# Kernel optimization log

Measured on AMD Instinct MI355X. Metric: run time of the kernel, lower is better.

The kernel has to match this reference:

```python
import jax, jax.numpy as jnp
import numpy as np

B, J, C = 256, 21, 256   # batch, joints, in_dim
H, D = 8, 256            # heads, out_dim (=hidden)
L, K = 2, 8              # layers, knn_k


def _knn_idx(coords, k):
    # coords: (B,J,3). Squared distances give same ordering as cdist p=2.
    d2 = jnp.sum((coords[:, :, None, :] - coords[:, None, :, :]) ** 2, axis=-1)  # (B,J,J)
    order = jnp.argsort(d2, axis=-1)
    return order[..., 1:k + 1]  # drop self -> (B,J,K)


def _mhgat(x, nbr_idx, wq, wk, wv, wp):
    b, j, _ = x.shape
    q = (x @ wq).reshape(b, j, H, D)
    k = (x @ wk).reshape(b, j, H, D)
    v = (x @ wv).reshape(b, j, H, D)
    bi = jnp.arange(b)[:, None, None]
    k_nbr = k[bi, nbr_idx]  # (B,J,K,H,D) gather of neighbor keys
    v_nbr = v[bi, nbr_idx]  # (B,J,K,H,D)
    attn = jnp.einsum('bjhd,bjkhd->bjkh', q, k_nbr) / np.float32(np.sqrt(D))
    attn = jax.nn.leaky_relu(attn, negative_slope=0.2)
    attn = jax.nn.softmax(attn, axis=2)  # over K neighbors
    out = jnp.einsum('bjkh,bjkhd->bjhd', attn, v_nbr).reshape(b, j, H * D)
    return out @ wp  # (B,J,hidden)


def setup_inputs() -> dict:
    key = jax.random.key(0)
    ks = jax.random.split(key, 9)
    s_in = 1.0 / np.sqrt(C)
    s_hd = 1.0 / np.sqrt(H * D)
    s_h = 1.0 / np.sqrt(D)
    joint_feats = jax.random.normal(ks[0], (B, J, C), jnp.float32)
    # layer-stacked weights (in_dim == hidden == 256 so both layers stack)
    wq = jax.random.normal(ks[1], (L, C, H * D), jnp.float32) * s_in
    wk = jax.random.normal(ks[2], (L, C, H * D), jnp.float32) * s_in
    wv = jax.random.normal(ks[3], (L, C, H * D), jnp.float32) * s_in
    wp = jax.random.normal(ks[4], (L, H * D, D), jnp.float32) * s_hd
    ws = jax.random.normal(ks[5], (L, C, D), jnp.float32) * s_in
    wskip0 = jax.random.normal(ks[6], (C, D), jnp.float32) * s_in
    fc_w = jax.random.normal(ks[7], (D, 3), jnp.float32) * s_h
    fc_b = jax.random.normal(ks[8], (3,), jnp.float32) * s_h
    return {"joint_feats": joint_feats, "wq": wq, "wk": wk, "wv": wv,
            "wp": wp, "ws": ws, "wskip0": wskip0, "fc_w": fc_w, "fc_b": fc_b}


def reference(joint_feats, wq, wk, wv, wp, ws, wskip0, fc_w, fc_b):
    h0 = joint_feats
    h = h0
    stats = []
    for l in range(L):
        nbr_idx = _knn_idx(jax.lax.stop_gradient(h[..., :3]), K)  # dynamic kNN graph
        out = _mhgat(h, nbr_idx, wq[l], wk[l], wv[l], wp[l])
        h = jax.nn.relu(out + h @ ws[l] + h0 @ wskip0)
        stats.append(jnp.abs(h).mean())
    coords = h @ fc_w + fc_b
    alphas = jnp.mean(jnp.stack(stats))
    return coords, alphas
```

## Files before the change

kernel.cpp:

```cpp
#include <hip/hip_runtime.h>
#include <hip/hip_bf16.h>
#include <math.h>
#include <type_traits>

namespace {
constexpr int Bb = 256, Jj = 21, Cc = 256, Hh = 8, Dd = 256;
constexpr int Mrows = Bb * Jj;
constexpr int HD    = Hh * Dd;
constexpr int QKVN  = 3 * HD;
constexpr int KNN   = 8;
constexpr int KFUSE = HD + Cc + Cc;

constexpr size_t OFF_QKV   = 0;
constexpr size_t OFF_T     = OFF_QKV   + (size_t)Mrows*QKVN*2;
constexpr size_t OFF_ATT   = OFF_T     + (size_t)Mrows*HD*4;
constexpr size_t OFF_GT    = OFF_ATT   + (size_t)Mrows*HD*2;
constexpr size_t OFF_JFB   = OFF_GT    + (size_t)HD*768*2;
constexpr size_t OFF_JFH   = OFF_JFB   + (size_t)Mrows*Cc*2;
constexpr size_t OFF_JFL   = OFF_JFH   + (size_t)Mrows*Cc*2;
constexpr size_t OFF_JFD   = OFF_JFL   + (size_t)Mrows*Cc*2;
constexpr size_t OFF_H1B   = OFF_JFD   + (size_t)Mrows*Cc*2;
constexpr size_t OFF_H2F   = OFF_H1B   + (size_t)Mrows*Cc*2;
constexpr size_t OFF_WQKVT = OFF_H2F   + (size_t)Mrows*Cc*4;
constexpr size_t OFF_FBT   = OFF_WQKVT + (size_t)2*QKVN*Cc*2;
constexpr size_t OFF_WVP   = OFF_FBT   + (size_t)2*Cc*KFUSE*2;
constexpr size_t OFF_VPROJ = OFF_WVP   + (size_t)Cc*24*4;
constexpr size_t OFF_WSUM  = OFF_VPROJ + (size_t)Mrows*24*4;
constexpr size_t OFF_CRD   = OFF_WSUM  + (size_t)Cc*4*4;
constexpr size_t OFF_NBR0  = OFF_CRD   + (size_t)Mrows*4*4;
constexpr size_t OFF_NBR1  = OFF_NBR0  + (size_t)Mrows*KNN*4;
constexpr size_t OFF_STAT  = OFF_NBR1  + (size_t)Mrows*KNN*4;
}

typedef short short8 __attribute__((ext_vector_type(8)));
typedef _Float16 half8 __attribute__((ext_vector_type(8)));
typedef _Float16 half4v __attribute__((ext_vector_type(4)));
typedef unsigned short u16x8 __attribute__((ext_vector_type(8)));
typedef float f32x4 __attribute__((ext_vector_type(4)));

__device__ __forceinline__ unsigned short f2bf(float x) {
    unsigned int u = __float_as_uint(x);
    u = u + 0x7fffu + ((u >> 16) & 1u);
    return (unsigned short)(u >> 16);
}
__device__ __forceinline__ float bf2f(unsigned short b) {
    return __uint_as_float(((unsigned int)b) << 16);
}

__device__ __forceinline__ void knn_body(int b, const float* __restrict__ src,
                                         int ld, int* __restrict__ nbr,
                                         float (*cs)[3]) {
    int t = threadIdx.x;
    if (t < Jj) {
        const float* p = src + (size_t)(b * Jj + t) * ld;
        cs[t][0] = p[0]; cs[t][1] = p[1]; cs[t][2] = p[2];
    }
    __syncthreads();
    if (t < Jj) {
        float x = cs[t][0], y = cs[t][1], z = cs[t][2];
        float d2[Jj];
        #pragma unroll
        for (int jj = 0; jj < Jj; ++jj) {
            float dx = x - cs[jj][0], dy = y - cs[jj][1], dz = z - cs[jj][2];
            d2[jj] = dx*dx + dy*dy + dz*dz;
        }
        unsigned int used = 0u;
        int out_base = (b * Jj + t) * KNN;
        #pragma unroll
        for (int r = 0; r <= KNN; ++r) {
            int best = -1; float bd = INFINITY;
            #pragma unroll
            for (int jj = 0; jj < Jj; ++jj)
                if (!((used >> jj) & 1u) && d2[jj] < bd) { bd = d2[jj]; best = jj; }
            used |= (1u << best);
            if (r > 0) nbr[out_base + r - 1] = best;
        }
    }
}

__global__ __launch_bounds__(256)
void mega_prep_kernel(const float* __restrict__ jf,
                      const float* __restrict__ wq, const float* __restrict__ wk,
                      const float* __restrict__ wv, const float* __restrict__ wp,
                      const float* __restrict__ wsw, const float* __restrict__ wsk,
                      unsigned short* __restrict__ wqkvT,
                      unsigned short* __restrict__ fbt, float* __restrict__ stats,
                      float* __restrict__ wsum,
                      unsigned short* __restrict__ jfb, _Float16* __restrict__ jfh,
                      _Float16* __restrict__ jfl, _Float16* __restrict__ jfd,
                      _Float16* __restrict__ GT, float* __restrict__ Wvp2,
                      int* __restrict__ nbr0) {
    __shared__ __align__(16) char sm[17408];
    int bid = blockIdx.x;
    int tidx = threadIdx.x;

    if (bid < 256) {
        int h = bid >> 5, rem = bid & 31;
        int m0 = (rem >> 2) * 32, n0 = (rem & 3) * 64;
        float (*As)[36] = (float(*)[36])sm;
        float (*Ws)[68] = (float(*)[68])(sm + 4608);
        int ty = tidx >> 4, tx = tidx & 15;
        float acc[2][4] = {};
        for (int kb = 0; kb < 256; kb += 32) {
            {
                int row = tidx >> 3, col = (tidx & 7) * 4;
                float4 v = *(const float4*)&wq[(size_t)(m0 + row)*HD + h*256 + kb + col];
                As[col+0][row] = v.x; As[col+1][row] = v.y;
                As[col+2][row] = v.z; As[col+3][row] = v.w;
                int row2 = tidx >> 2, col2 = (tidx & 3) * 8;
                float4 u0 = *(const float4*)&wk[(size_t)(n0 + row2)*HD + h*256 + kb + col2];
                float4 u1 = *(const float4*)&wk[(size_t)(n0 + row2)*HD + h*256 + kb + col2 + 4];
                Ws[col2+0][row2] = u0.x; Ws[col2+1][row2] = u0.y;
                Ws[col2+2][row2] = u0.z; Ws[col2+3][row2] = u0.w;
                Ws[col2+4][row2] = u1.x; Ws[col2+5][row2] = u1.y;
                Ws[col2+6][row2] = u1.z; Ws[col2+7][row2] = u1.w;
            }
            __syncthreads();
            #pragma unroll
            for (int kk = 0; kk < 32; ++kk) {
                float a0 = As[kk][ty*2], a1 = As[kk][ty*2 + 1];
                float4 bv = *(const float4*)&Ws[kk][tx*4];
                float b4[4] = {bv.x, bv.y, bv.z, bv.w};
                #pragma unroll
                for (int j = 0; j < 4; ++j) {
                    acc[0][j] += a0 * b4[j];
                    acc[1][j] += a1 * b4[j];
                }
            }
            __syncthreads();
        }
        #pragma unroll
        for (int j = 0; j < 4; ++j) {
            int n = h*256 + n0 + tx*4 + j;
            float g0 = acc[0][j], g1 = acc[1][j];
            _Float16 h0_ = (_Float16)g0, h1_ = (_Float16)g1;
            _Float16* base = &GT[(size_t)n*768 + m0 + ty*2];
            base[0]   = h0_;                          base[1]   = h1_;
            base[256] = (_Float16)(g0 * 0.0625f);     base[257] = (_Float16)(g1 * 0.0625f);
            base[512] = (_Float16)((g0 - (float)h0_) * 128.0f);
            base[513] = (_Float16)((g1 - (float)h1_) * 128.0f);
        }
    } else if (bid < 264) {
        int h = bid - 256;
        float (*wpc)[3] = (float(*)[3])sm;
        int t = tidx;
        const float* p = &wp[(size_t)(h*256 + t) * Cc];
        wpc[t][0] = p[0]; wpc[t][1] = p[1]; wpc[t][2] = p[2];
        __syncthreads();
        const float* vr = &wv[(size_t)t*HD + h*256];
        float a0=0, a1=0, a2=0;
        for (int d = 0; d < 256; ++d) {
            float v = vr[d];
            a0 += v*wpc[d][0]; a1 += v*wpc[d][1]; a2 += v*wpc[d][2];
        }
        float* o = &Wvp2[(size_t)t*24 + h*3];
        o[0]=a0; o[1]=a1; o[2]=a2;
    } else if (bid < 520) {
        knn_body(bid - 264, jf, Cc, nbr0, (float(*)[3])sm);
    } else if (bid == 520) {
        int e = tidx;
        float4 o;
        o.x = wsw[(size_t)e*Dd + 0] + wsk[(size_t)e*Dd + 0];
        o.y = wsw[(size_t)e*Dd + 1] + wsk[(size_t)e*Dd + 1];
        o.z = wsw[(size_t)e*Dd + 2] + wsk[(size_t)e*Dd + 2];
        o.w = 0.0f;
        *(float4*)&wsum[e*4] = o;
        if (e < 2) stats[e] = 0.0f;
    } else if (bid < 1865) {
        int i = (bid - 521) * 256 + tidx;
        float4 v = ((const float4*)jf)[i];
        float x[4] = {v.x, v.y, v.z, v.w};
        ushort4 ob; half4v oh, ol, od;
        #pragma unroll
        for (int u = 0; u < 4; ++u) {
            ((unsigned short*)&ob)[u] = f2bf(x[u]);
            _Float16 h = (_Float16)x[u];
            oh[u] = h;
            ol[u] = (_Float16)((x[u] - (float)h) * 16.0f);
            od[u] = (_Float16)(x[u] * 0.0078125f);
        }
        ((ushort4*)jfb)[i] = ob;
        ((half4v*)jfh)[i] = oh;
        ((half4v*)jfl)[i] = ol;
        ((half4v*)jfd)[i] = od;
    } else {
        int tt = bid - 1865;
        const float* src; unsigned short* dst;
        int ldin, ldout, tilesX, tile;
        constexpr size_t CH = (size_t)Cc * HD;
        if (tt < 3072) {
            int op = tt >> 9; tile = tt & 511; tilesX = 64;
            ldin = HD; ldout = Cc;
            const float* s3[3] = {wq, wk, wv};
            src = s3[op % 3] + (size_t)(op / 3) * CH;
            dst = wqkvT + (size_t)(op % 3) * HD * Cc + (size_t)(op / 3) * QKVN * Cc;
        } else if (tt < 4096) {
            int op = (tt - 3072) >> 9; tile = (tt - 3072) & 511; tilesX = 8;
            ldin = Cc; ldout = KFUSE;
            src = wp + (size_t)op * HD * Cc;
            dst = fbt + (size_t)op * Cc * KFUSE;
        } else {
            int q = tt - 4096; int op = q >> 6; tile = q & 63; tilesX = 8;
            ldin = Cc; ldout = KFUSE;
            const float* s4[4] = {wsw, wsw + (size_t)Cc * Cc, wsk, wsk};
            src = s4[op];
            dst = fbt + (size_t)(op & 1) * Cc * KFUSE + HD + (size_t)(op >> 1) * Cc;
        }
        int bx = tile % tilesX, by = tile / tilesX;
        int n0 = bx * 32, k0 = by * 32;
        float (*t)[33] = (float(*)[33])sm;
        int r = tidx >> 3, c4 = (tidx & 7) * 4;
        float4 v = *(const float4*)&src[(size_t)(k0 + r) * ldin + n0 + c4];
        t[r][c4+0] = v.x; t[r][c4+1] = v.y; t[r][c4+2] = v.z; t[r][c4+3] = v.w;
        __syncthreads();
        ushort4 o;
        o.x = f2bf(t[c4+0][r]); o.y = f2bf(t[c4+1][r]);
        o.z = f2bf(t[c4+2][r]); o.w = f2bf(t[c4+3][r]);
        *(ushort4*)&dst[(size_t)(n0 + r) * ldout + k0 + c4] = o;
    }
}

template<int BM, int BN, int BK, int NSEG, bool RELU_STATS, bool OUT_BF16, bool F16>
__device__ __forceinline__
void gemm_core(unsigned short* As, unsigned short* Bs, float* red,
               int bm, int bn,
               const unsigned short* __restrict__ A0, int lda0, int klen0,
               const unsigned short* __restrict__ A1, int lda1, int klen1,
               const unsigned short* __restrict__ A2, int lda2, int klen2,
               const unsigned short* __restrict__ Bt, int ldb,
               void* __restrict__ Cv, int ldc, float* __restrict__ stat) {
    constexpr int WM = BM/2, WN = BN/2;
    constexpr int MW = WM/16, NW = WN/16, KW = BK/32;
    constexpr int CHUNKA = BM*BK/8;
    constexpr int CHUNKB = BN*BK/8;
    constexpr int KB8 = BK/8;
    constexpr int SWZ = KB8 - 1;
    using frag = std::conditional_t<F16, half8, short8>;

    int tid = threadIdx.x;
    int wid = tid >> 6, lane = tid & 63;
    int wr = wid >> 1, wc = wid & 1;

    f32x4 acc[MW][NW];
    #pragma unroll
    for (int m = 0; m < MW; ++m)
        #pragma unroll
        for (int n = 0; n < NW; ++n)
            acc[m][n] = (f32x4){0.f, 0.f, 0.f, 0.f};

    const unsigned short* Aseg[3] = {A0, A1, A2};
    const int ldas[3] = {lda0, lda1, lda2};
    const int klens[3] = {klen0, klen1, klen2};

    int kglob = 0;
    for (int seg = 0; seg < NSEG; ++seg) {
        const unsigned short* A = Aseg[seg];
        const int lda = ldas[seg];
        const int klen = klens[seg];
        for (int k0 = 0; k0 < klen; k0 += BK) {
            #pragma unroll
            for (int it = 0; it < CHUNKA/256; ++it) {
                int c = tid + it*256;
                int row = c / KB8;
                int kp = (c % KB8) ^ (row & SWZ);
                __builtin_amdgcn_global_load_lds(
                    (const __attribute__((address_space(1))) unsigned int*)
                        (A + (size_t)(bm + row)*lda + k0 + kp*8),
                    (__attribute__((address_space(3))) unsigned int*)(As + c*8),
                    16, 0, 0);
            }
            #pragma unroll
            for (int it = 0; it < CHUNKB/256; ++it) {
                int c = tid + it*256;
                int row = c / KB8;
                int kp = (c % KB8) ^ (row & SWZ);
                __builtin_amdgcn_global_load_lds(
                    (const __attribute__((address_space(1))) unsigned int*)
                        (Bt + (size_t)(bn + row)*ldb + kglob + k0 + kp*8),
                    (__attribute__((address_space(3))) unsigned int*)(Bs + c*8),
                    16, 0, 0);
            }
            __syncthreads();
            #pragma unroll
            for (int kp = 0; kp < KW; ++kp) {
                frag af[MW], bf[NW];
                int cbase = kp*4 + (lane >> 4);
                #pragma unroll
                for (int m = 0; m < MW; ++m) {
                    int r = wr*WM + m*16 + (lane & 15);
                    af[m] = *(const frag*)&As[r*BK + ((cbase ^ (r & SWZ))*8)];
                }
                #pragma unroll
                for (int n = 0; n < NW; ++n) {
                    int r = wc*WN + n*16 + (lane & 15);
                    bf[n] = *(const frag*)&Bs[r*BK + ((cbase ^ (r & SWZ))*8)];
                }
                #pragma unroll
                for (int m = 0; m < MW; ++m)
                    #pragma unroll
                    for (int n = 0; n < NW; ++n) {
                        if constexpr (F16)
                            acc[m][n] = __builtin_amdgcn_mfma_f32_16x16x32_f16(
                                af[m], bf[n], acc[m][n], 0, 0, 0);
                        else
                            acc[m][n] = __builtin_amdgcn_mfma_f32_16x16x32_bf16(
                                af[m], bf[n], acc[m][n], 0, 0, 0);
                    }
            }
            __syncthreads();
        }
        kglob += klen;
    }

    int cr = (lane >> 4)*4, cc = lane & 15;
    float bsum = 0.0f;
    #pragma unroll
    for (int m = 0; m < MW; ++m)
        #pragma unroll
        for (int n = 0; n < NW; ++n)
            #pragma unroll
            for (int j = 0; j < 4; ++j) {
                float v = acc[m][n][j];
                if (RELU_STATS) { v = fmaxf(v, 0.0f); bsum += v; }
                size_t row = bm + wr*WM + m*16 + cr + j;
                size_t col = bn + wc*WN + n*16 + cc;
                if (OUT_BF16) ((unsigned short*)Cv)[row*ldc + col] = f2bf(v);
                else          ((float*)Cv)[row*ldc + col] = v;
            }
    if (RELU_STATS) {
        #pragma unroll
        for (int sft = 1; sft < 64; sft <<= 1) bsum += __shfl_xor(bsum, sft);
        if (lane == 0) red[wid] = bsum;
        __syncthreads();
        if (tid == 0) atomicAdd(stat, red[0] + red[1] + red[2] + red[3]);
    }
}

__global__ __launch_bounds__(256)
void combo_kernel(const unsigned short* __restrict__ jfb,
                  const unsigned short* __restrict__ wqkvT,
                  unsigned short* __restrict__ QKVb,
                  const _Float16* __restrict__ jfh, const _Float16* __restrict__ jfl,
                  const _Float16* __restrict__ jfd, const _Float16* __restrict__ GT,
                  float* __restrict__ Tm,
                  const float* __restrict__ jf, const float* __restrict__ Wvp2,
                  float* __restrict__ vproj) {
    __shared__ __align__(16) char smem[32784];
    unsigned short* As = (unsigned short*)smem;
    unsigned short* Bs = (unsigned short*)(smem + 16384);
    float* red = (float*)(smem + 32768);
    int x = blockIdx.x, y = blockIdx.y;
    if (y < 16) {
        int lb = x + 42*y;
        int nb = (lb & 7) * 84 + (lb >> 3);
        int sx = nb % 42, sy = nb / 42;
        gemm_core<128,128,64,1,false,true,false>(As, Bs, red, sx*128,
            2*HD + sy*128,
            jfb, Cc, Cc, jfb, Cc, 0, jfb, Cc, 0, wqkvT, Cc, QKVb, QKVN, nullptr);
    } else if (y < 32) {
        int lb = x + 42*(y - 16);
        int nb = (lb & 7) * 84 + (lb >> 3);
        int sx = nb / 16, sy = nb % 16;
        gemm_core<128,128,64,3,false,false,true>(As, Bs, red, sx*128, sy*128,
            (const unsigned short*)jfh, Cc, Cc, (const unsigned short*)jfl, Cc, Cc,
            (const unsigned short*)jfd, Cc, Cc, (const unsigned short*)GT, 768,
            Tm, HD, nullptr);
    } else {
        int q = (y - 32) * 42 + x;
        float (*hr)[256] = (float(*)[256])smem;
        float* wl = (float*)(smem + 8192);
        int t = threadIdx.x;
        int j0 = q * 8;
        #pragma unroll
        for (int i = 0; i < 6; ++i)
            *(float4*)&wl[t*4 + i*1024] = *(const float4*)&Wvp2[t*4 + i*1024];
        {
            int r = t >> 5, c = (t & 31) * 8;
            const float* src = &jf[(size_t)(j0 + r)*Cc + c];
            *(float4*)&hr[r][c]   = *(const float4*)src;
            *(float4*)&hr[r][c+4] = *(const float4*)(src + 4);
        }
        __syncthreads();
        int r = t >> 5, o = t & 31;
        if (o < 24) {
            float a = 0.0f;
            for (int e = 0; e < 256; ++e) a += hr[r][e] * wl[e*24 + o];
            vproj[(size_t)(j0 + r)*24 + o] = a;
        }
    }
}

__global__ __launch_bounds__(256)
void qkv1_kernel(const unsigned short* __restrict__ h1b,
                 const unsigned short* __restrict__ wqkvT1,
                 unsigned short* __restrict__ QKVb) {
    __shared__ __align__(16) unsigned short As[128*64];
    __shared__ __align__(16) unsigned short Bs[128*64];
    __shared__ float red[4];
    int lb = blockIdx.x + 42*blockIdx.y;
    int nb = (lb & 7) * 252 + (lb >> 3);
    int sx = nb % 42, sy = nb / 42;
    gemm_core<128,128,64,1,false,true,false>(
        As, Bs, red, sx*128, sy*128,
        h1b, Cc, Cc, h1b, Cc, 0, h1b, Cc, 0, wqkvT1, Cc, QKVb, QKVN, nullptr);
}

template<bool OUT_BF16, bool DO_KNN>
__global__ __launch_bounds__(256)
void fused_kernel(const unsigned short* __restrict__ att,
                  const unsigned short* __restrict__ hseg,
                  const unsigned short* __restrict__ h0seg,
                  const unsigned short* __restrict__ fbtL,
                  void* __restrict__ Cv, float* __restrict__ stat,
                  const float* __restrict__ crd, int* __restrict__ nbr1) {
    __shared__ __align__(16) char smem[16400];
    if (DO_KNN && blockIdx.y >= 4) {
        int b = (blockIdx.y - 4) * 84 + blockIdx.x;
        if (b < Bb) knn_body(b, crd, 4, nbr1, (float(*)[3])smem);
        return;
    }
    unsigned short* As = (unsigned short*)smem;
    unsigned short* Bs = (unsigned short*)(smem + 8192);
    float* red = (float*)(smem + 16384);
    gemm_core<64,64,64,3,true,OUT_BF16,false>(
        As, Bs, red, blockIdx.x*64, blockIdx.y*64,
        att, HD, HD, hseg, Cc, Cc, h0seg, Cc, Cc,
        fbtL, KFUSE, Cv, Cc, stat);
}

__global__ __launch_bounds__(64)
void precise_kernel(const float* __restrict__ T, const float* __restrict__ h0,
                    const int* __restrict__ nbr, const float* __restrict__ vproj,
                    const float* __restrict__ wsum,
                    const unsigned short* __restrict__ QKV,
                    float* __restrict__ crd, unsigned short* __restrict__ att) {
    int lb = blockIdx.x;
    int i = (lb & 7) * (Mrows/8) + (lb >> 3);
    int b = i / Jj;
    int l = threadIdx.x;
    __shared__ float Ts[8][260];
    __shared__ float nb[8][260];
    __shared__ float hi[256];
    __shared__ float wsL[64];
    __shared__ int nbs[KNN];
    #pragma unroll
    for (int u = 0; u < 8; ++u) {
        int idx = u*64 + l;
        float4 v = *(const float4*)&T[(size_t)i*HD + idx*4];
        int hh = idx >> 6, dd = (idx & 63) * 4;
        *(float4*)&Ts[hh][dd] = v;
    }
    *(float4*)&hi[l*4] = *(const float4*)&h0[(size_t)i*Cc + l*4];
    if (l < KNN) nbs[l] = nbr[i*KNN + l];
    int kq = l >> 3, s = l & 7;
    int njs = nbr[i*KNN + kq];
    const float* nrow = &h0[(size_t)(b*Jj + njs)*Cc];
    #pragma unroll
    for (int u = 0; u < 8; ++u)
        *(float4*)&nb[kq][(s*8+u)*4] = *(const float4*)&nrow[(s*8+u)*4];
    __syncthreads();

    int k = l >> 3, h = l & 7;
    float sacc = 0;
    #pragma unroll 8
    for (int d = 0; d < 256; d += 4) {
        float4 tv = *(const float4*)&Ts[h][d];
        float4 nv = *(const float4*)&nb[k][d];
        sacc += tv.x*nv.x + tv.y*nv.y + tv.z*nv.z + tv.w*nv.w;
    }
    float sc = sacc * 0.0625f;
    sc = (sc >= 0.0f) ? sc : 0.2f * sc;
    float m = sc;
    m = fmaxf(m, __shfl_xor(m, 8));
    m = fmaxf(m, __shfl_xor(m, 16));
    m = fmaxf(m, __shfl_xor(m, 32));
    float e = expf(sc - m);
    float den = e;
    den += __shfl_xor(den, 8); den += __shfl_xor(den, 16); den += __shfl_xor(den, 32);
    float w = e / den;
    wsL[l] = w;

    int njk = nbs[k];
    const float* vp = &vproj[(size_t)(b*Jj + njk)*24 + h*3];
    float t0 = w * vp[0], t1 = w * vp[1], t2 = w * vp[2];
    #pragma unroll
    for (int u = 0; u < 4; ++u) {
        int e4 = l*4 + u;
        float hv = hi[e4];
        float4 wv = *(const float4*)&wsum[e4*4];
        t0 += hv * wv.x; t1 += hv * wv.y; t2 += hv * wv.z;
    }
    #pragma unroll
    for (int sft = 1; sft < 64; sft <<= 1) {
        t0 += __shfl_xor(t0, sft); t1 += __shfl_xor(t1, sft); t2 += __shfl_xor(t2, sft);
    }
    if (l == 0) {
        crd[i*4+0] = fmaxf(t0, 0.0f);
        crd[i*4+1] = fmaxf(t1, 0.0f);
        crd[i*4+2] = fmaxf(t2, 0.0f);
        crd[i*4+3] = 0.0f;
    }
    __syncthreads();

    int h2 = l >> 3, sub = l & 7;
    float o[32] = {};
    #pragma unroll
    for (int kk = 0; kk < KNN; ++kk) {
        float wk_ = wsL[kk*8 + h2];
        const unsigned short* vrow =
            &QKV[(size_t)(b*Jj + nbs[kk])*QKVN + 2*HD + h2*256 + sub*32];
        #pragma unroll
        for (int j = 0; j < 4; ++j) {
            u16x8 v = *(const u16x8*)(vrow + j*8);
            #pragma unroll
            for (int u = 0; u < 8; ++u) o[j*8+u] += wk_ * bf2f(v[u]);
        }
    }
    unsigned short* arow = &att[(size_t)i*HD + h2*256 + sub*32];
    #pragma unroll
    for (int j = 0; j < 4; ++j) {
        u16x8 ou;
        #pragma unroll
        for (int u = 0; u < 8; ++u) ou[u] = f2bf(o[j*8+u]);
        *(u16x8*)(arow + j*8) = ou;
    }
}

__global__ __launch_bounds__(64)
void attn_kernel(const unsigned short* __restrict__ QKV,
                 const int* __restrict__ nbr, unsigned short* __restrict__ att) {
    int lb = blockIdx.x;
    int gid = (lb & 7) * (Mrows*4/8) + (lb >> 3);
    int hp = gid & 3, row = gid >> 2, b = row / Jj;
    int lane = threadIdx.x;
    int h = hp*2 + (lane >> 5);
    int d0 = (lane & 31) * 8;

    u16x8 qu = *(const u16x8*)&QKV[(size_t)row*QKVN + h*Dd + d0];
    float qf[8];
    #pragma unroll
    for (int i = 0; i < 8; ++i) qf[i] = bf2f(qu[i]);
    const int* np_ = nbr + row * KNN;

    float sc[KNN]; int nb[KNN];
    #pragma unroll
    for (int k = 0; k < KNN; ++k) {
        int n = np_[k]; nb[k] = n;
        u16x8 ku = *(const u16x8*)&QKV[(size_t)(b*Jj + n)*QKVN + HD + h*Dd + d0];
        float p = 0;
        #pragma unroll
        for (int i = 0; i < 8; ++i) p += qf[i] * bf2f(ku[i]);
        #pragma unroll
        for (int s = 1; s < 32; s <<= 1) p += __shfl_xor(p, s);
        sc[k] = p;
    }
    float mx = -INFINITY;
    #pragma unroll
    for (int k = 0; k < KNN; ++k) {
        float s = sc[k] * 0.0625f;
        s = (s >= 0.0f) ? s : 0.2f * s;
        sc[k] = s; mx = fmaxf(mx, s);
    }
    float den = 0.0f;
    #pragma unroll
    for (int k = 0; k < KNN; ++k) { sc[k] = expf(sc[k] - mx); den += sc[k]; }
    float inv = 1.0f / den;
    float o[8] = {};
    #pragma unroll
    for (int k = 0; k < KNN; ++k) {
        u16x8 vu = *(const u16x8*)&QKV[(size_t)(b*Jj + nb[k])*QKVN + 2*HD + h*Dd + d0];
        float w = sc[k] * inv;
        #pragma unroll
        for (int i = 0; i < 8; ++i) o[i] += w * bf2f(vu[i]);
    }
    u16x8 ou;
    #pragma unroll
    for (int i = 0; i < 8; ++i) ou[i] = f2bf(o[i]);
    *(u16x8*)&att[(size_t)row*HD + h*Dd + d0] = ou;
}

__global__ __launch_bounds__(64)
void final_kernel(const float* __restrict__ h, const float* __restrict__ fcw,
                  const float* __restrict__ fcb, const float* __restrict__ stats,
                  float* __restrict__ out) {
    int row = blockIdx.x, lane = threadIdx.x;
    const float4 hv = *(const float4*)(h + (size_t)row*Cc + lane*4);
    float a0=0, a1=0, a2=0;
    const float hx[4] = {hv.x, hv.y, hv.z, hv.w};
    #pragma unroll
    for (int i = 0; i < 4; ++i) {
        int c = lane*4 + i;
        a0 += hx[i]*fcw[c*3+0]; a1 += hx[i]*fcw[c*3+1]; a2 += hx[i]*fcw[c*3+2];
    }
    #pragma unroll
    for (int s = 32; s > 0; s >>= 1) {
        a0 += __shfl_xor(a0, s); a1 += __shfl_xor(a1, s); a2 += __shfl_xor(a2, s);
    }
    if (lane == 0) {
        out[row*3+0] = a0 + fcb[0];
        out[row*3+1] = a1 + fcb[1];
        out[row*3+2] = a2 + fcb[2];
        if (row == 0)
            out[(size_t)Mrows*3] =
                (stats[0] + stats[1]) * (0.5f / ((float)Mrows * (float)Cc));
    }
}

extern "C" void kernel_launch(void* const* d_in, const int* in_sizes, int n_in,
                              void* d_out, int out_size, void* d_ws, size_t ws_size,
                              hipStream_t stream) {
    (void)in_sizes; (void)n_in; (void)out_size; (void)ws_size;
    const float* jf     = (const float*)d_in[0];
    const float* wq     = (const float*)d_in[1];
    const float* wk     = (const float*)d_in[2];
    const float* wv     = (const float*)d_in[3];
    const float* wp     = (const float*)d_in[4];
    const float* wsw    = (const float*)d_in[5];
    const float* wskip0 = (const float*)d_in[6];
    const float* fcw    = (const float*)d_in[7];
    const float* fcb    = (const float*)d_in[8];
    float* out = (float*)d_out;

    char* wsb = (char*)d_ws;
    unsigned short* QKVb  = (unsigned short*)(wsb + OFF_QKV);
    float*          Tm    = (float*)(wsb + OFF_T);
    unsigned short* attb  = (unsigned short*)(wsb + OFF_ATT);
    _Float16*       GT    = (_Float16*)(wsb + OFF_GT);
    unsigned short* jfb   = (unsigned short*)(wsb + OFF_JFB);
    _Float16*       jfh   = (_Float16*)(wsb + OFF_JFH);
    _Float16*       jfl   = (_Float16*)(wsb + OFF_JFL);
    _Float16*       jfd   = (_Float16*)(wsb + OFF_JFD);
    unsigned short* h1b   = (unsigned short*)(wsb + OFF_H1B);
    float*          h2f   = (float*)(wsb + OFF_H2F);
    unsigned short* wqkvT = (unsigned short*)(wsb + OFF_WQKVT);
    unsigned short* fbt   = (unsigned short*)(wsb + OFF_FBT);
    float*          Wvp   = (float*)(wsb + OFF_WVP);
    float*          vproj = (float*)(wsb + OFF_VPROJ);
    float*          wsum  = (float*)(wsb + OFF_WSUM);
    float*          crd   = (float*)(wsb + OFF_CRD);
    int*            nbr0  = (int*)(wsb + OFF_NBR0);
    int*            nbr1  = (int*)(wsb + OFF_NBR1);
    float*          stats = (float*)(wsb + OFF_STAT);

    mega_prep_kernel<<<6217, 256, 0, stream>>>(jf, wq, wk, wv, wp, wsw, wskip0,
                                               wqkvT, fbt, stats, wsum,
                                               jfb, jfh, jfl, jfd, GT, Wvp, nbr0);
    combo_kernel<<<dim3(42, 48), 256, 0, stream>>>(jfb, wqkvT, QKVb,
                                                   jfh, jfl, jfd, GT, Tm,
                                                   jf, Wvp, vproj);
    precise_kernel<<<Mrows, 64, 0, stream>>>(Tm, jf, nbr0, vproj, wsum,
                                             QKVb, crd, attb);
    fused_kernel<true, true><<<dim3(84, 8), 256, 0, stream>>>(
        attb, jfb, jfb, fbt, h1b, &stats[0], crd, nbr1);
    qkv1_kernel<<<dim3(42, 48), 256, 0, stream>>>(h1b, wqkvT + (size_t)QKVN*Cc, QKVb);
    attn_kernel<<<Mrows*4, 64, 0, stream>>>(QKVb, nbr1, attb);
    fused_kernel<false, false><<<dim3(84, 4), 256, 0, stream>>>(
        attb, h1b, jfb, fbt + (size_t)Cc*KFUSE, h2f, &stats[1], nullptr, nullptr);
    final_kernel<<<Mrows, 64, 0, stream>>>(h2f, fcw, fcb, stats, out);
}
```

Before: 194.6 us.

## Fold layer-1 query-key product into precomputed Wq·Wkᵀ to skip K projection

For layer 1, the prep kernel now precomputes per-head G1 = Wq_h·Wk_hᵀ in bf16, and the layer-1 GEMM computes T = h1·G1 in place of Q and K. The attention kernel then dots T with neighbor h1 rows directly. This removes the separate K projection and the wide bf16 K reads in attention, cutting GEMM work by a third for that layer. The cost is extra weight-prep GEMM blocks and rounding G1 to bf16, which may change accuracy.

New measurement: 191.5 us. About the same (-1.6%).

```diff
diff --git a/kernel.cpp b/kernel.cpp
--- a/kernel.cpp
+++ b/kernel.cpp
@@ -15,7 +15,8 @@
 constexpr size_t OFF_T     = OFF_QKV   + (size_t)Mrows*QKVN*2;
 constexpr size_t OFF_ATT   = OFF_T     + (size_t)Mrows*HD*4;
 constexpr size_t OFF_GT    = OFF_ATT   + (size_t)Mrows*HD*2;
-constexpr size_t OFF_JFB   = OFF_GT    + (size_t)HD*768*2;
+constexpr size_t OFF_G1T   = OFF_GT    + (size_t)HD*768*2;
+constexpr size_t OFF_JFB   = OFF_G1T   + (size_t)HD*Cc*2;
 constexpr size_t OFF_JFH   = OFF_JFB   + (size_t)Mrows*Cc*2;
 constexpr size_t OFF_JFL   = OFF_JFH   + (size_t)Mrows*Cc*2;
 constexpr size_t OFF_JFD   = OFF_JFL   + (size_t)Mrows*Cc*2;
@@ -78,6 +79,44 @@
     }
 }
 
+__device__ __forceinline__ void g_gemm_body(const float* __restrict__ wq,
+                                            const float* __restrict__ wk,
+                                            int h, int m0, int n0, char* sm,
+                                            float acc[2][4]) {
+    float (*As)[36] = (float(*)[36])sm;
+    float (*Ws)[68] = (float(*)[68])(sm + 4608);
+    int tidx = threadIdx.x;
+    int ty = tidx >> 4, tx = tidx & 15;
+    for (int kb = 0; kb < 256; kb += 32) {
+        {
+            int row = tidx >> 3, col = (tidx & 7) * 4;
+            float4 v = *(const float4*)&wq[(size_t)(m0 + row)*HD + h*256 + kb + col];
+            As[col+0][row] = v.x; As[col+1][row] = v.y;
+            As[col+2][row] = v.z; As[col+3][row] = v.w;
+            int row2 = tidx >> 2, col2 = (tidx & 3) * 8;
+            float4 u0 = *(const float4*)&wk[(size_t)(n0 + row2)*HD + h*256 + kb + col2];
+            float4 u1 = *(const float4*)&wk[(size_t)(n0 + row2)*HD + h*256 + kb + col2 + 4];
+            Ws[col2+0][row2] = u0.x; Ws[col2+1][row2] = u0.y;
+            Ws[col2+2][row2] = u0.z; Ws[col2+3][row2] = u0.w;
+            Ws[col2+4][row2] = u1.x; Ws[col2+5][row2] = u1.y;
+            Ws[col2+6][row2] = u1.z; Ws[col2+7][row2] = u1.w;
+        }
+        __syncthreads();
+        #pragma unroll
+        for (int kk = 0; kk < 32; ++kk) {
+            float a0 = As[kk][ty*2], a1 = As[kk][ty*2 + 1];
+            float4 bv = *(const float4*)&Ws[kk][tx*4];
+            float b4[4] = {bv.x, bv.y, bv.z, bv.w};
+            #pragma unroll
+            for (int j = 0; j < 4; ++j) {
+                acc[0][j] += a0 * b4[j];
+                acc[1][j] += a1 * b4[j];
+            }
+        }
+        __syncthreads();
+    }
+}
+
 __global__ __launch_bounds__(256)
 void mega_prep_kernel(const float* __restrict__ jf,
                       const float* __restrict__ wq, const float* __restrict__ wk,
@@ -88,47 +127,19 @@
                       float* __restrict__ wsum,
                       unsigned short* __restrict__ jfb, _Float16* __restrict__ jfh,
                       _Float16* __restrict__ jfl, _Float16* __restrict__ jfd,
-                      _Float16* __restrict__ GT, float* __restrict__ Wvp2,
-                      int* __restrict__ nbr0) {
+                      _Float16* __restrict__ GT, unsigned short* __restrict__ G1T,
+                      float* __restrict__ Wvp2, int* __restrict__ nbr0) {
     __shared__ __align__(16) char sm[17408];
     int bid = blockIdx.x;
     int tidx = threadIdx.x;
+    constexpr size_t CH = (size_t)Cc * HD;
 
     if (bid < 256) {
         int h = bid >> 5, rem = bid & 31;
         int m0 = (rem >> 2) * 32, n0 = (rem & 3) * 64;
-        float (*As)[36] = (float(*)[36])sm;
-        float (*Ws)[68] = (float(*)[68])(sm + 4608);
         int ty = tidx >> 4, tx = tidx & 15;
         float acc[2][4] = {};
-        for (int kb = 0; kb < 256; kb += 32) {
-            {
-                int row = tidx >> 3, col = (tidx & 7) * 4;
-                float4 v = *(const float4*)&wq[(size_t)(m0 + row)*HD + h*256 + kb + col];
-                As[col+0][row] = v.x; As[col+1][row] = v.y;
-                As[col+2][row] = v.z; As[col+3][row] = v.w;
-                int row2 = tidx >> 2, col2 = (tidx & 3) * 8;
-                float4 u0 = *(const float4*)&wk[(size_t)(n0 + row2)*HD + h*256 + kb + col2];
-                float4 u1 = *(const float4*)&wk[(size_t)(n0 + row2)*HD + h*256 + kb + col2 + 4];
-                Ws[col2+0][row2] = u0.x; Ws[col2+1][row2] = u0.y;
-                Ws[col2+2][row2] = u0.z; Ws[col2+3][row2] = u0.w;
-                Ws[col2+4][row2] = u1.x; Ws[col2+5][row2] = u1.y;
-                Ws[col2+6][row2] = u1.z; Ws[col2+7][row2] = u1.w;
-            }
-            __syncthreads();
-            #pragma unroll
-            for (int kk = 0; kk < 32; ++kk) {
-                float a0 = As[kk][ty*2], a1 = As[kk][ty*2 + 1];
-                float4 bv = *(const float4*)&Ws[kk][tx*4];
-                float b4[4] = {bv.x, bv.y, bv.z, bv.w};
-                #pragma unroll
-                for (int j = 0; j < 4; ++j) {
-                    acc[0][j] += a0 * b4[j];
-                    acc[1][j] += a1 * b4[j];
-                }
-            }
-            __syncthreads();
-        }
+        g_gemm_body(wq, wk, h, m0, n0, sm, acc);
         #pragma unroll
         for (int j = 0; j < 4; ++j) {
             int n = h*256 + n0 + tx*4 + j;
@@ -140,8 +151,22 @@
             base[512] = (_Float16)((g0 - (float)h0_) * 128.0f);
             base[513] = (_Float16)((g1 - (float)h1_) * 128.0f);
         }
-    } else if (bid < 264) {
-        int h = bid - 256;
+    } else if (bid < 512) {
+        int q = bid - 256;
+        int h = q >> 5, rem = q & 31;
+        int m0 = (rem >> 2) * 32, n0 = (rem & 3) * 64;
+        int ty = tidx >> 4, tx = tidx & 15;
+        float acc[2][4] = {};
+        g_gemm_body(wq + CH, wk + CH, h, m0, n0, sm, acc);
+        #pragma unroll
+        for (int j = 0; j < 4; ++j) {
+            int n = h*256 + n0 + tx*4 + j;
+            unsigned short* base = &G1T[(size_t)n*256 + m0 + ty*2];
+            base[0] = f2bf(acc[0][j]);
+            base[1] = f2bf(acc[1][j]);
+        }
+    } else if (bid < 520) {
+        int h = bid - 512;
         float (*wpc)[3] = (float(*)[3])sm;
         int t = tidx;
         const float* p = &wp[(size_t)(h*256 + t) * Cc];
@@ -155,9 +180,9 @@
         }
         float* o = &Wvp2[(size_t)t*24 + h*3];
         o[0]=a0; o[1]=a1; o[2]=a2;
-    } else if (bid < 520) {
-        knn_body(bid - 264, jf, Cc, nbr0, (float(*)[3])sm);
-    } else if (bid == 520) {
+    } else if (bid < 776) {
+        knn_body(bid - 520, jf, Cc, nbr0, (float(*)[3])sm);
+    } else if (bid == 776) {
         int e = tidx;
         float4 o;
         o.x = wsw[(size_t)e*Dd + 0] + wsk[(size_t)e*Dd + 0];
@@ -166,8 +191,8 @@
         o.w = 0.0f;
         *(float4*)&wsum[e*4] = o;
         if (e < 2) stats[e] = 0.0f;
-    } else if (bid < 1865) {
-        int i = (bid - 521) * 256 + tidx;
+    } else if (bid < 2121) {
+        int i = (bid - 777) * 256 + tidx;
         float4 v = ((const float4*)jf)[i];
         float x[4] = {v.x, v.y, v.z, v.w};
         ushort4 ob; half4v oh, ol, od;
@@ -184,23 +209,23 @@
         ((half4v*)jfl)[i] = ol;
         ((half4v*)jfd)[i] = od;
     } else {
-        int tt = bid - 1865;
+        int tt = bid - 2121;
         const float* src; unsigned short* dst;
         int ldin, ldout, tilesX, tile;
-        constexpr size_t CH = (size_t)Cc * HD;
-        if (tt < 3072) {
-            int op = tt >> 9; tile = tt & 511; tilesX = 64;
+        if (tt < 2048) {
+            int opIdx = tt >> 9; tile = tt & 511; tilesX = 64;
+            int op = (opIdx < 3) ? opIdx : 5;
             ldin = HD; ldout = Cc;
             const float* s3[3] = {wq, wk, wv};
             src = s3[op % 3] + (size_t)(op / 3) * CH;
             dst = wqkvT + (size_t)(op % 3) * HD * Cc + (size_t)(op / 3) * QKVN * Cc;
-        } else if (tt < 4096) {
-            int op = (tt - 3072) >> 9; tile = (tt - 3072) & 511; tilesX = 8;
+        } else if (tt < 3072) {
+            int op = (tt - 2048) >> 9; tile = (tt - 2048) & 511; tilesX = 8;
             ldin = Cc; ldout = KFUSE;
             src = wp + (size_t)op * HD * Cc;
             dst = fbt + (size_t)op * Cc * KFUSE;
         } else {
-            int q = tt - 4096; int op = q >> 6; tile = q & 63; tilesX = 8;
+            int q = tt - 3072; int op = q >> 6; tile = q & 63; tilesX = 8;
             ldin = Cc; ldout = KFUSE;
             const float* s4[4] = {wsw, wsw + (size_t)Cc * Cc, wsk, wsk};
             src = s4[op];
@@ -391,18 +416,28 @@
 }
 
 __global__ __launch_bounds__(256)
-void qkv1_kernel(const unsigned short* __restrict__ h1b,
-                 const unsigned short* __restrict__ wqkvT1,
-                 unsigned short* __restrict__ QKVb) {
+void combo1_kernel(const unsigned short* __restrict__ h1b,
+                   const unsigned short* __restrict__ wqkvT1,
+                   const unsigned short* __restrict__ G1T,
+                   unsigned short* __restrict__ QKVb) {
     __shared__ __align__(16) unsigned short As[128*64];
     __shared__ __align__(16) unsigned short Bs[128*64];
     __shared__ float red[4];
-    int lb = blockIdx.x + 42*blockIdx.y;
-    int nb = (lb & 7) * 252 + (lb >> 3);
-    int sx = nb % 42, sy = nb / 42;
-    gemm_core<128,128,64,1,false,true,false>(
-        As, Bs, red, sx*128, sy*128,
-        h1b, Cc, Cc, h1b, Cc, 0, h1b, Cc, 0, wqkvT1, Cc, QKVb, QKVN, nullptr);
+    int x = blockIdx.x, y = blockIdx.y;
+    if (y < 16) {
+        int lb = x + 42*y;
+        int nb = (lb & 7) * 84 + (lb >> 3);
+        int sx = nb % 42, sy = nb / 42;
+        gemm_core<128,128,64,1,false,true,false>(As, Bs, red, sx*128,
+            2*HD + sy*128,
+            h1b, Cc, Cc, h1b, Cc, 0, h1b, Cc, 0, wqkvT1, Cc, QKVb, QKVN, nullptr);
+    } else {
+        int lb = x + 42*(y - 16);
+        int nb = (lb & 7) * 84 + (lb >> 3);
+        int sx = nb % 42, sy = nb / 42;
+        gemm_core<128,128,64,1,false,true,false>(As, Bs, red, sx*128, sy*128,
+            h1b, Cc, Cc, h1b, Cc, 0, h1b, Cc, 0, G1T, Cc, QKVb, QKVN, nullptr);
+    }
 }
 
 template<bool OUT_BF16, bool DO_KNN>
@@ -527,8 +562,9 @@
 }
 
 __global__ __launch_bounds__(64)
-void attn_kernel(const unsigned short* __restrict__ QKV,
-                 const int* __restrict__ nbr, unsigned short* __restrict__ att) {
+void attn1_kernel(const unsigned short* __restrict__ QKV,
+                  const unsigned short* __restrict__ h1b,
+                  const int* __restrict__ nbr, unsigned short* __restrict__ att) {
     int lb = blockIdx.x;
     int gid = (lb & 7) * (Mrows*4/8) + (lb >> 3);
     int hp = gid & 3, row = gid >> 2, b = row / Jj;
@@ -536,20 +572,20 @@
     int h = hp*2 + (lane >> 5);
     int d0 = (lane & 31) * 8;
 
-    u16x8 qu = *(const u16x8*)&QKV[(size_t)row*QKVN + h*Dd + d0];
-    float qf[8];
-    #pragma unroll
-    for (int i = 0; i < 8; ++i) qf[i] = bf2f(qu[i]);
+    u16x8 tu = *(const u16x8*)&QKV[(size_t)row*QKVN + h*Dd + d0];
+    float tf[8];
+    #pragma unroll
+    for (int i = 0; i < 8; ++i) tf[i] = bf2f(tu[i]);
     const int* np_ = nbr + row * KNN;
 
     float sc[KNN]; int nb[KNN];
     #pragma unroll
     for (int k = 0; k < KNN; ++k) {
         int n = np_[k]; nb[k] = n;
-        u16x8 ku = *(const u16x8*)&QKV[(size_t)(b*Jj + n)*QKVN + HD + h*Dd + d0];
+        u16x8 hu = *(const u16x8*)&h1b[(size_t)(b*Jj + n)*Cc + d0];
         float p = 0;
         #pragma unroll
-        for (int i = 0; i < 8; ++i) p += qf[i] * bf2f(ku[i]);
+        for (int i = 0; i < 8; ++i) p += tf[i] * bf2f(hu[i]);
         #pragma unroll
         for (int s = 1; s < 32; s <<= 1) p += __shfl_xor(p, s);
         sc[k] = p;
@@ -626,6 +662,7 @@
     float*          Tm    = (float*)(wsb + OFF_T);
     unsigned short* attb  = (unsigned short*)(wsb + OFF_ATT);
     _Float16*       GT    = (_Float16*)(wsb + OFF_GT);
+    unsigned short* G1T   = (unsigned short*)(wsb + OFF_G1T);
     unsigned short* jfb   = (unsigned short*)(wsb + OFF_JFB);
     _Float16*       jfh   = (_Float16*)(wsb + OFF_JFH);
     _Float16*       jfl   = (_Float16*)(wsb + OFF_JFL);
@@ -642,9 +679,10 @@
     int*            nbr1  = (int*)(wsb + OFF_NBR1);
     float*          stats = (float*)(wsb + OFF_STAT);
 
-    mega_prep_kernel<<<6217, 256, 0, stream>>>(jf, wq, wk, wv, wp, wsw, wskip0,
+    mega_prep_kernel<<<5449, 256, 0, stream>>>(jf, wq, wk, wv, wp, wsw, wskip0,
                                                wqkvT, fbt, stats, wsum,
-                                               jfb, jfh, jfl, jfd, GT, Wvp, nbr0);
+                                               jfb, jfh, jfl, jfd, GT, G1T,
+                                               Wvp, nbr0);
     combo_kernel<<<dim3(42, 48), 256, 0, stream>>>(jfb, wqkvT, QKVb,
                                                    jfh, jfl, jfd, GT, Tm,
                                                    jf, Wvp, vproj);
@@ -652,8 +690,9 @@
                                              QKVb, crd, attb);
     fused_kernel<true, true><<<dim3(84, 8), 256, 0, stream>>>(
         attb, jfb, jfb, fbt, h1b, &stats[0], crd, nbr1);
-    qkv1_kernel<<<dim3(42, 48), 256, 0, stream>>>(h1b, wqkvT + (size_t)QKVN*Cc, QKVb);
-    attn_kernel<<<Mrows*4, 64, 0, stream>>>(QKVb, nbr1, attb);
+    combo1_kernel<<<dim3(42, 32), 256, 0, stream>>>(
+        h1b, wqkvT + (size_t)QKVN*Cc, G1T, QKVb);
+    attn1_kernel<<<Mrows*4, 64, 0, stream>>>(QKVb, h1b, nbr1, attb);
     fused_kernel<false, false><<<dim3(84, 4), 256, 0, stream>>>(
         attb, h1b, jfb, fbt + (size_t)Cc*KFUSE, h2f, &stats[1], nullptr, nullptr);
     final_kernel<<<Mrows, 64, 0, stream>>>(h2f, fcw, fcb, stats, out);
```
